# Kernel tuning notes

Measured on AMD Instinct MI355X. Metric: run time of the kernel, lower is better.

The kernel has to match this reference:

```python
import jax, jax.numpy as jnp
import numpy as np

D_MODEL = 2048
D_STATE = 16
BATCH = 2048

def setup_inputs() -> dict:
    key = jax.random.key(0)
    ks = jax.random.split(key, 8)
    x_t = jax.random.normal(ks[0], (BATCH, D_MODEL), dtype=jnp.float32)
    ssm_state_prev = jax.random.normal(ks[1], (BATCH, D_MODEL, D_STATE), dtype=jnp.float32)
    # parameters (match torch init semantics loosely; values random)
    A_log = jnp.log(jnp.tile(jnp.arange(1, D_STATE + 1, dtype=jnp.float32)[None, :], (D_MODEL, 1)))
    s = 1.0 / np.sqrt(D_MODEL)
    W_B = jax.random.uniform(ks[2], (D_STATE, D_MODEL), minval=-s, maxval=s, dtype=jnp.float32)
    W_C = jax.random.uniform(ks[3], (D_STATE, D_MODEL), minval=-s, maxval=s, dtype=jnp.float32)
    W_Delta = jax.random.uniform(ks[4], (D_MODEL, D_MODEL), minval=-s, maxval=s, dtype=jnp.float32)
    b_Delta = jax.random.uniform(ks[5], (D_MODEL,), minval=-s, maxval=s, dtype=jnp.float32)
    D_param = jnp.ones((D_MODEL,), dtype=jnp.float32)
    return {"x_t": x_t, "ssm_state_prev": ssm_state_prev, "A_log": A_log,
            "W_B": W_B, "W_C": W_C, "W_Delta": W_Delta, "b_Delta": b_Delta,
            "D_param": D_param}

def reference(x_t, ssm_state_prev, A_log, W_B, W_C, W_Delta, b_Delta, D_param):
    A = -jnp.exp(A_log)                         # (d_model, d_state)
    B_t = x_t @ W_B.T                            # (B, d_state)
    C_t = x_t @ W_C.T                            # (B, d_state)
    Delta_t = jax.nn.softplus(x_t @ W_Delta.T + b_Delta)   # (B, d_model)
    A_bar = jnp.exp(Delta_t[:, :, None] * A[None, :, :])   # (B, d_model, d_state)
    Delta_B = Delta_t[:, :, None] * B_t[:, None, :]         # (B, d_model, d_state)
    ssm_state_t = A_bar * ssm_state_prev + Delta_B * x_t[:, :, None]
    y_t = jnp.sum(ssm_state_t * C_t[:, None, :], axis=-1) + D_param * x_t
    return (y_t, ssm_state_t)
```

## Files before the change

kernel.cpp:

```cpp
#include <hip/hip_runtime.h>

#define D_MODEL 2048
#define D_STATE 16
#define BATCH   2048

typedef __attribute__((ext_vector_type(8))) short bf16x8;
typedef __attribute__((ext_vector_type(4))) float f32x4;
typedef __attribute__((ext_vector_type(8))) unsigned short u16x8;

__device__ __forceinline__ unsigned short f2bf(float f) {
  unsigned u = __float_as_uint(f);
  u = (u + 0x7FFFu + ((u >> 16) & 1u)) >> 16;
  return (unsigned short)u;
}

__device__ __forceinline__ void cvt8(const float* __restrict__ s, unsigned short* __restrict__ d) {
  f32x4 a = *(const f32x4*)s;
  f32x4 b = *(const f32x4*)(s + 4);
  u16x8 o;
  o[0] = f2bf(a[0]); o[1] = f2bf(a[1]); o[2] = f2bf(a[2]); o[3] = f2bf(a[3]);
  o[4] = f2bf(b[0]); o[5] = f2bf(b[1]); o[6] = f2bf(b[2]); o[7] = f2bf(b[3]);
  *(u16x8*)d = o;
}

__global__ __launch_bounds__(256) void prep_kernel(
    const float* __restrict__ x, const float* __restrict__ wd,
    const float* __restrict__ wb, const float* __restrict__ wc,
    const float* __restrict__ alog,
    unsigned short* __restrict__ x_bf, unsigned short* __restrict__ w_bf,
    unsigned short* __restrict__ wbc, float* __restrict__ nA) {
  int t = blockIdx.x * 256 + threadIdx.x;
  if (t < 524288) {
    cvt8(x + t * 8, x_bf + t * 8);
  } else if (t < 1048576) {
    int i = (t - 524288) * 8;
    cvt8(wd + i, w_bf + i);
  } else if (t < 1081344) {
    int i = (t - 1048576) * 8;
    int row = i >> 11, col = i & 2047;
    if (row < 16)      cvt8(wb + row * 2048 + col, wbc + i);
    else if (row < 32) cvt8(wc + (row - 16) * 2048 + col, wbc + i);
    else { u16x8 z = {0,0,0,0,0,0,0,0}; *(u16x8*)(wbc + i) = z; }
  } else {
    int i = (t - 1081344) * 4;
    f32x4 v = *(const f32x4*)(alog + i);
    f32x4 o;
    o[0] = __expf(v[0]); o[1] = __expf(v[1]); o[2] = __expf(v[2]); o[3] = __expf(v[3]);
    *(f32x4*)(nA + i) = o;
  }
}

__global__ __launch_bounds__(256) void gemm_kernel(
    const unsigned short* __restrict__ Abf,
    const unsigned short* __restrict__ Wbf,
    const unsigned short* __restrict__ WBC,
    const float* __restrict__ bias,
    float* __restrict__ Delta,
    float* __restrict__ BC) {
  __shared__ __align__(16) unsigned short lA[2][8192];
  __shared__ __align__(16) unsigned short lB[2][8192];

  const int tid = threadIdx.x;
  const bool isBC = (blockIdx.y == 16);
  const int brow = blockIdx.x * 128;
  const int bcol = isBC ? 0 : blockIdx.y * 128;
  const unsigned short* Bsrc = isBC ? WBC : (Wbf + (size_t)bcol * 2048);
  const unsigned short* Asrc = Abf + (size_t)brow * 2048;

  const int lane = tid & 63;
  const int wid = tid >> 6;
  const int wr = wid >> 1, wcid = wid & 1;
  const int fr = lane & 15;
  const int kg = lane >> 4;

  int srcoff[4];
#pragma unroll
  for (int i = 0; i < 4; ++i) {
    int ci = i * 256 + tid;
    int r = ci >> 3, cs = ci & 7;
    int c = cs ^ (r & 7);
    srcoff[i] = r * 2048 + c * 8;
  }
  const int ldsb = (tid >> 6) << 10;

  f32x4 acc[4][4];
#pragma unroll
  for (int m = 0; m < 4; ++m)
#pragma unroll
    for (int n = 0; n < 4; ++n) acc[m][n] = (f32x4){0.f, 0.f, 0.f, 0.f};

#define STAGE(buf, k0)                                                          \
  do {                                                                          \
    _Pragma("unroll")                                                           \
    for (int i = 0; i < 4; ++i)                                                 \
      __builtin_amdgcn_global_load_lds(                                         \
          (const __attribute__((address_space(1))) void*)(Asrc + (size_t)srcoff[i] + (k0)), \
          (__attribute__((address_space(3))) void*)((char*)lA[buf] + i * 4096 + ldsb), \
          16, 0, 0);                                                            \
    _Pragma("unroll")                                                           \
    for (int i = 0; i < 4; ++i)                                                 \
      __builtin_amdgcn_global_load_lds(                                         \
          (const __attribute__((address_space(1))) void*)(Bsrc + (size_t)srcoff[i] + (k0)), \
          (__attribute__((address_space(3))) void*)((char*)lB[buf] + i * 4096 + ldsb), \
          16, 0, 0);                                                            \
  } while (0)

  STAGE(0, 0);
  asm volatile("s_waitcnt vmcnt(0)" ::: "memory");
  __builtin_amdgcn_s_barrier();
  int cur = 0;
#pragma unroll 1
  for (int t = 0; t < 32; ++t) {
    if (t < 31) STAGE(cur ^ 1, (t + 1) * 64);

    bf16x8 fa[2][4], fb[2][4];
#pragma unroll
    for (int m = 0; m < 4; ++m) {
      int row = wr * 64 + m * 16 + fr;
#pragma unroll
      for (int kk = 0; kk < 2; ++kk)
        fa[kk][m] = *(const bf16x8*)((const char*)lA[cur] + row * 128 +
                                     ((((kk << 2) + kg) ^ (row & 7)) << 4));
    }
#pragma unroll
    for (int n = 0; n < 4; ++n) {
      int row = wcid * 64 + n * 16 + fr;
#pragma unroll
      for (int kk = 0; kk < 2; ++kk)
        fb[kk][n] = *(const bf16x8*)((const char*)lB[cur] + row * 128 +
                                     ((((kk << 2) + kg) ^ (row & 7)) << 4));
    }
#pragma unroll
    for (int kk = 0; kk < 2; ++kk)
#pragma unroll
      for (int m = 0; m < 4; ++m)
#pragma unroll
        for (int n = 0; n < 4; ++n)
          acc[m][n] = __builtin_amdgcn_mfma_f32_16x16x32_bf16(fa[kk][m], fb[kk][n], acc[m][n], 0, 0, 0);

    asm volatile("s_waitcnt vmcnt(0)" ::: "memory");
    __builtin_amdgcn_s_barrier();
    cur ^= 1;
  }
#undef STAGE

  const int rq = kg * 4;
#pragma unroll
  for (int m = 0; m < 4; ++m) {
    int grow = brow + wr * 64 + m * 16 + rq;
#pragma unroll
    for (int n = 0; n < 4; ++n) {
      int gcol = bcol + wcid * 64 + n * 16 + fr;
      if (!isBC) {
        float bv = bias[gcol];
#pragma unroll
        for (int q = 0; q < 4; ++q) {
          float v = acc[m][n][q] + bv;
          v = fmaxf(v, 0.f) + log1pf(__expf(-fabsf(v)));
          Delta[(size_t)(grow + q) * 2048 + gcol] = v;
        }
      } else {
#pragma unroll
        for (int q = 0; q < 4; ++q)
          BC[(size_t)(grow + q) * 128 + gcol] = acc[m][n][q];
      }
    }
  }
}

__global__ __launch_bounds__(256) void pointwise_kernel(
    const float* __restrict__ x, const float* __restrict__ sp,
    const float* __restrict__ nA, const float* __restrict__ BCb,
    const float* __restrict__ Delta, const float* __restrict__ Dp,
    float* __restrict__ y, float* __restrict__ st) {
  int t = blockIdx.x * 256 + threadIdx.x;
  int sg = t & 1;
  int d = (t >> 1) & 2047;
  int b = t >> 12;
  int bd = (b << 11) + d;
  float delta = Delta[bd];
  float xv = x[bd];
  float dx = delta * xv;
  const f32x4* spp = (const f32x4*)sp + ((size_t)t << 1);
  f32x4 s0 = __builtin_nontemporal_load(spp);
  f32x4 s1 = __builtin_nontemporal_load(spp + 1);
  const f32x4* ap = (const f32x4*)nA + ((d << 2) + (sg << 1));
  f32x4 a0 = ap[0], a1 = ap[1];
  const f32x4* bp = (const f32x4*)BCb + ((b << 5) + (sg << 1));
  f32x4 b0 = bp[0], b1 = bp[1];
  f32x4 c0 = bp[4], c1 = bp[5];
  f32x4 r0, r1;
  r0[0] = __expf(-delta * a0[0]) * s0[0] + dx * b0[0];
  r0[1] = __expf(-delta * a0[1]) * s0[1] + dx * b0[1];
  r0[2] = __expf(-delta * a0[2]) * s0[2] + dx * b0[2];
  r0[3] = __expf(-delta * a0[3]) * s0[3] + dx * b0[3];
  r1[0] = __expf(-delta * a1[0]) * s1[0] + dx * b1[0];
  r1[1] = __expf(-delta * a1[1]) * s1[1] + dx * b1[1];
  r1[2] = __expf(-delta * a1[2]) * s1[2] + dx * b1[2];
  r1[3] = __expf(-delta * a1[3]) * s1[3] + dx * b1[3];
  f32x4* stp = (f32x4*)st + ((size_t)t << 1);
  __builtin_nontemporal_store(r0, stp);
  __builtin_nontemporal_store(r1, stp + 1);
  float p = r0[0] * c0[0] + r0[1] * c0[1] + r0[2] * c0[2] + r0[3] * c0[3]
          + r1[0] * c1[0] + r1[1] * c1[1] + r1[2] * c1[2] + r1[3] * c1[3];
  p += __shfl_xor(p, 1, 2);
  if (sg == 0) y[bd] = p + Dp[d] * xv;
}

extern "C" void kernel_launch(void* const* d_in, const int* in_sizes, int n_in,
                              void* d_out, int out_size, void* d_ws, size_t ws_size,
                              hipStream_t stream) {
  const float* x    = (const float*)d_in[0];
  const float* sp   = (const float*)d_in[1];
  const float* alog = (const float*)d_in[2];
  const float* wb   = (const float*)d_in[3];
  const float* wc   = (const float*)d_in[4];
  const float* wd   = (const float*)d_in[5];
  const float* bdel = (const float*)d_in[6];
  const float* dp   = (const float*)d_in[7];
  float* y  = (float*)d_out;
  float* st = (float*)d_out + (size_t)BATCH * D_MODEL;

  char* ws = (char*)d_ws;
  unsigned short* x_bf = (unsigned short*)ws;
  unsigned short* w_bf = (unsigned short*)(ws + 8388608);
  unsigned short* wbc  = (unsigned short*)(ws + 16777216);
  float* Delta = (float*)(ws + 17301504);
  float* BC    = (float*)(ws + 34078720);
  float* nA    = (float*)(ws + 35127296);

  prep_kernel<<<4256, 256, 0, stream>>>(x, wd, wb, wc, alog, x_bf, w_bf, wbc, nA);
  gemm_kernel<<<dim3(16, 17), 256, 0, stream>>>(x_bf, w_bf, wbc, bdel, Delta, BC);
  pointwise_kernel<<<32768, 256, 0, stream>>>(x, sp, nA, BC, Delta, dp, y, st);
}
```

Baseline: 547.4 us.

## Fuse SSM pointwise update into GEMM epilogue and compute B/C projections in prep

```diff
diff --git a/kernel.cpp b/kernel.cpp
--- a/kernel.cpp
+++ b/kernel.cpp
@@ -28,44 +28,58 @@
     const float* __restrict__ wb, const float* __restrict__ wc,
     const float* __restrict__ alog,
     unsigned short* __restrict__ x_bf, unsigned short* __restrict__ w_bf,
-    unsigned short* __restrict__ wbc, float* __restrict__ nA) {
-  int t = blockIdx.x * 256 + threadIdx.x;
-  if (t < 524288) {
-    cvt8(x + t * 8, x_bf + t * 8);
-  } else if (t < 1048576) {
-    int i = (t - 524288) * 8;
+    float* __restrict__ nA, float* __restrict__ BCg) {
+  const int bid = blockIdx.x, tid = threadIdx.x;
+  if (bid < 2048) {
+    int i = (bid * 256 + tid) * 8;
+    cvt8(x + i, x_bf + i);
+  } else if (bid < 4096) {
+    int i = ((bid - 2048) * 256 + tid) * 8;
     cvt8(wd + i, w_bf + i);
-  } else if (t < 1081344) {
-    int i = (t - 1048576) * 8;
-    int row = i >> 11, col = i & 2047;
-    if (row < 16)      cvt8(wb + row * 2048 + col, wbc + i);
-    else if (row < 32) cvt8(wc + (row - 16) * 2048 + col, wbc + i);
-    else { u16x8 z = {0,0,0,0,0,0,0,0}; *(u16x8*)(wbc + i) = z; }
-  } else {
-    int i = (t - 1081344) * 4;
+  } else if (bid < 4128) {
+    int i = ((bid - 4096) * 256 + tid) * 4;
     f32x4 v = *(const f32x4*)(alog + i);
     f32x4 o;
     o[0] = __expf(v[0]); o[1] = __expf(v[1]); o[2] = __expf(v[2]); o[3] = __expf(v[3]);
     *(f32x4*)(nA + i) = o;
-  }
-}
-
-__global__ __launch_bounds__(256) void gemm_kernel(
+  } else {
+    int bci = bid - 4128;
+    int r = bci * 16 + (tid >> 4);
+    int j0 = (tid & 15) * 2;
+    const float* xr = x + (size_t)r * 2048;
+    const float* w0 = (j0 < 16) ? (wb + j0 * 2048) : (wc + (j0 - 16) * 2048);
+    const float* w1 = (j0 + 1 < 16) ? (wb + (j0 + 1) * 2048) : (wc + (j0 - 15) * 2048);
+    f32x4 a0 = (f32x4){0.f, 0.f, 0.f, 0.f}, a1 = a0;
+    for (int k = 0; k < 2048; k += 4) {
+      f32x4 xv = *(const f32x4*)(xr + k);
+      a0 += xv * *(const f32x4*)(w0 + k);
+      a1 += xv * *(const f32x4*)(w1 + k);
+    }
+    BCg[(size_t)r * 32 + j0]     = a0[0] + a0[1] + a0[2] + a0[3];
+    BCg[(size_t)r * 32 + j0 + 1] = a1[0] + a1[1] + a1[2] + a1[3];
+  }
+}
+
+#define LDSA(buf) ((unsigned short*)(smem + (buf) * 16384))
+#define LDSB(buf) ((unsigned short*)(smem + 32768 + (buf) * 16384))
+
+__global__ __launch_bounds__(256) void fused_kernel(
     const unsigned short* __restrict__ Abf,
     const unsigned short* __restrict__ Wbf,
-    const unsigned short* __restrict__ WBC,
     const float* __restrict__ bias,
-    float* __restrict__ Delta,
-    float* __restrict__ BC) {
-  __shared__ __align__(16) unsigned short lA[2][8192];
-  __shared__ __align__(16) unsigned short lB[2][8192];
+    const float* __restrict__ nAg,
+    const float* __restrict__ BCg,
+    const float* __restrict__ xg,
+    const float* __restrict__ sp,
+    const float* __restrict__ Dp,
+    float* __restrict__ y, float* __restrict__ st) {
+  __shared__ __align__(16) unsigned char smem[65536];
 
   const int tid = threadIdx.x;
-  const bool isBC = (blockIdx.y == 16);
   const int brow = blockIdx.x * 128;
-  const int bcol = isBC ? 0 : blockIdx.y * 128;
-  const unsigned short* Bsrc = isBC ? WBC : (Wbf + (size_t)bcol * 2048);
+  const int bcol = blockIdx.y * 128;
   const unsigned short* Asrc = Abf + (size_t)brow * 2048;
+  const unsigned short* Bsrc = Wbf + (size_t)bcol * 2048;
 
   const int lane = tid & 63;
   const int wid = tid >> 6;
@@ -95,13 +109,13 @@
     for (int i = 0; i < 4; ++i)                                                 \
       __builtin_amdgcn_global_load_lds(                                         \
           (const __attribute__((address_space(1))) void*)(Asrc + (size_t)srcoff[i] + (k0)), \
-          (__attribute__((address_space(3))) void*)((char*)lA[buf] + i * 4096 + ldsb), \
+          (__attribute__((address_space(3))) void*)((char*)LDSA(buf) + i * 4096 + ldsb), \
           16, 0, 0);                                                            \
     _Pragma("unroll")                                                           \
     for (int i = 0; i < 4; ++i)                                                 \
       __builtin_amdgcn_global_load_lds(                                         \
           (const __attribute__((address_space(1))) void*)(Bsrc + (size_t)srcoff[i] + (k0)), \
-          (__attribute__((address_space(3))) void*)((char*)lB[buf] + i * 4096 + ldsb), \
+          (__attribute__((address_space(3))) void*)((char*)LDSB(buf) + i * 4096 + ldsb), \
           16, 0, 0);                                                            \
   } while (0)
 
@@ -119,7 +133,7 @@
       int row = wr * 64 + m * 16 + fr;
 #pragma unroll
       for (int kk = 0; kk < 2; ++kk)
-        fa[kk][m] = *(const bf16x8*)((const char*)lA[cur] + row * 128 +
+        fa[kk][m] = *(const bf16x8*)((const char*)LDSA(cur) + row * 128 +
                                      ((((kk << 2) + kg) ^ (row & 7)) << 4));
     }
 #pragma unroll
@@ -127,7 +141,7 @@
       int row = wcid * 64 + n * 16 + fr;
 #pragma unroll
       for (int kk = 0; kk < 2; ++kk)
-        fb[kk][n] = *(const bf16x8*)((const char*)lB[cur] + row * 128 +
+        fb[kk][n] = *(const bf16x8*)((const char*)LDSB(cur) + row * 128 +
                                      ((((kk << 2) + kg) ^ (row & 7)) << 4));
     }
 #pragma unroll
@@ -144,67 +158,86 @@
   }
 #undef STAGE
 
-  const int rq = kg * 4;
+  float bvn[4], dpn[4];
+#pragma unroll
+  for (int n = 0; n < 4; ++n) {
+    int gcol = bcol + wcid * 64 + n * 16 + fr;
+    bvn[n] = bias[gcol];
+    dpn[n] = Dp[gcol];
+  }
+#pragma unroll
+  for (int m = 0; m < 4; ++m)
+#pragma unroll
+    for (int n = 0; n < 4; ++n)
+#pragma unroll
+      for (int q = 0; q < 4; ++q) {
+        float v = acc[m][n][q] + bvn[n];
+        acc[m][n][q] = fmaxf(v, 0.f) + log1pf(__expf(-fabsf(v)));
+      }
+
+  __syncthreads();
+  float* bc_lds = (float*)smem;
+  float* na_lds = (float*)(smem + 16384);
+  {
+    const f32x4* src = (const f32x4*)(BCg + (size_t)brow * 32);
+#pragma unroll
+    for (int i = 0; i < 4; ++i) ((f32x4*)bc_lds)[tid + i * 256] = src[tid + i * 256];
+    const float* ns = nAg + (size_t)bcol * 16;
+#pragma unroll
+    for (int i = 0; i < 8; ++i) {
+      int idx = tid + i * 256;
+      na_lds[(idx >> 4) * 20 + (idx & 15)] = ns[idx];
+    }
+  }
+  __syncthreads();
+
+  f32x4 na_reg[4][4];
+#pragma unroll
+  for (int n = 0; n < 4; ++n) {
+    const float* np = na_lds + (wcid * 64 + n * 16 + fr) * 20;
+#pragma unroll
+    for (int s = 0; s < 4; ++s) na_reg[n][s] = *(const f32x4*)(np + s * 4);
+  }
+
 #pragma unroll
   for (int m = 0; m < 4; ++m) {
-    int grow = brow + wr * 64 + m * 16 + rq;
-#pragma unroll
-    for (int n = 0; n < 4; ++n) {
-      int gcol = bcol + wcid * 64 + n * 16 + fr;
-      if (!isBC) {
-        float bv = bias[gcol];
-#pragma unroll
-        for (int q = 0; q < 4; ++q) {
-          float v = acc[m][n][q] + bv;
-          v = fmaxf(v, 0.f) + log1pf(__expf(-fabsf(v)));
-          Delta[(size_t)(grow + q) * 2048 + gcol] = v;
+#pragma unroll
+    for (int q = 0; q < 4; ++q) {
+      int bloc = wr * 64 + m * 16 + (kg << 2) + q;
+      int bglob = brow + bloc;
+      const float* bcp = bc_lds + bloc * 32;
+      f32x4 bt[4], ct[4];
+#pragma unroll
+      for (int s = 0; s < 4; ++s) {
+        bt[s] = *(const f32x4*)(bcp + s * 4);
+        ct[s] = *(const f32x4*)(bcp + 16 + s * 4);
+      }
+      size_t rowbase = (size_t)bglob << 11;
+#pragma unroll
+      for (int n = 0; n < 4; ++n) {
+        int dglob = bcol + wcid * 64 + n * 16 + fr;
+        float delta = acc[m][n][q];
+        float xv = xg[rowbase + dglob];
+        float dx = delta * xv;
+        const f32x4* spp = (const f32x4*)sp + ((rowbase + dglob) << 2);
+        f32x4* stp = (f32x4*)st + ((rowbase + dglob) << 2);
+        float psum = 0.f;
+#pragma unroll
+        for (int s = 0; s < 4; ++s) {
+          f32x4 sv = __builtin_nontemporal_load(spp + s);
+          f32x4 av = na_reg[n][s];
+          f32x4 r;
+          r[0] = __expf(-delta * av[0]) * sv[0] + dx * bt[s][0];
+          r[1] = __expf(-delta * av[1]) * sv[1] + dx * bt[s][1];
+          r[2] = __expf(-delta * av[2]) * sv[2] + dx * bt[s][2];
+          r[3] = __expf(-delta * av[3]) * sv[3] + dx * bt[s][3];
+          __builtin_nontemporal_store(r, stp + s);
+          psum += r[0] * ct[s][0] + r[1] * ct[s][1] + r[2] * ct[s][2] + r[3] * ct[s][3];
         }
-      } else {
-#pragma unroll
-        for (int q = 0; q < 4; ++q)
-          BC[(size_t)(grow + q) * 128 + gcol] = acc[m][n][q];
+        y[rowbase + dglob] = psum + dpn[n] * xv;
       }
     }
   }
-}
-
-__global__ __launch_bounds__(256) void pointwise_kernel(
-    const float* __restrict__ x, const float* __restrict__ sp,
-    const float* __restrict__ nA, const float* __restrict__ BCb,
-    const float* __restrict__ Delta, const float* __restrict__ Dp,
-    float* __restrict__ y, float* __restrict__ st) {
-  int t = blockIdx.x * 256 + threadIdx.x;
-  int sg = t & 1;
-  int d = (t >> 1) & 2047;
-  int b = t >> 12;
-  int bd = (b << 11) + d;
-  float delta = Delta[bd];
-  float xv = x[bd];
-  float dx = delta * xv;
-  const f32x4* spp = (const f32x4*)sp + ((size_t)t << 1);
-  f32x4 s0 = __builtin_nontemporal_load(spp);
-  f32x4 s1 = __builtin_nontemporal_load(spp + 1);
-  const f32x4* ap = (const f32x4*)nA + ((d << 2) + (sg << 1));
-  f32x4 a0 = ap[0], a1 = ap[1];
-  const f32x4* bp = (const f32x4*)BCb + ((b << 5) + (sg << 1));
-  f32x4 b0 = bp[0], b1 = bp[1];
-  f32x4 c0 = bp[4], c1 = bp[5];
-  f32x4 r0, r1;
-  r0[0] = __expf(-delta * a0[0]) * s0[0] + dx * b0[0];
-  r0[1] = __expf(-delta * a0[1]) * s0[1] + dx * b0[1];
-  r0[2] = __expf(-delta * a0[2]) * s0[2] + dx * b0[2];
-  r0[3] = __expf(-delta * a0[3]) * s0[3] + dx * b0[3];
-  r1[0] = __expf(-delta * a1[0]) * s1[0] + dx * b1[0];
-  r1[1] = __expf(-delta * a1[1]) * s1[1] + dx * b1[1];
-  r1[2] = __expf(-delta * a1[2]) * s1[2] + dx * b1[2];
-  r1[3] = __expf(-delta * a1[3]) * s1[3] + dx * b1[3];
-  f32x4* stp = (f32x4*)st + ((size_t)t << 1);
-  __builtin_nontemporal_store(r0, stp);
-  __builtin_nontemporal_store(r1, stp + 1);
-  float p = r0[0] * c0[0] + r0[1] * c0[1] + r0[2] * c0[2] + r0[3] * c0[3]
-          + r1[0] * c1[0] + r1[1] * c1[1] + r1[2] * c1[2] + r1[3] * c1[3];
-  p += __shfl_xor(p, 1, 2);
-  if (sg == 0) y[bd] = p + Dp[d] * xv;
 }
 
 extern "C" void kernel_launch(void* const* d_in, const int* in_sizes, int n_in,
@@ -224,12 +257,9 @@
   char* ws = (char*)d_ws;
   unsigned short* x_bf = (unsigned short*)ws;
   unsigned short* w_bf = (unsigned short*)(ws + 8388608);
-  unsigned short* wbc  = (unsigned short*)(ws + 16777216);
-  float* Delta = (float*)(ws + 17301504);
-  float* BC    = (float*)(ws + 34078720);
-  float* nA    = (float*)(ws + 35127296);
-
-  prep_kernel<<<4256, 256, 0, stream>>>(x, wd, wb, wc, alog, x_bf, w_bf, wbc, nA);
-  gemm_kernel<<<dim3(16, 17), 256, 0, stream>>>(x_bf, w_bf, wbc, bdel, Delta, BC);
-  pointwise_kernel<<<32768, 256, 0, stream>>>(x, sp, nA, BC, Delta, dp, y, st);
-}
+  float* nA  = (float*)(ws + 16777216);
+  float* BCg = (float*)(ws + 16908288);
+
+  prep_kernel<<<4256, 256, 0, stream>>>(x, wd, wb, wc, alog, x_bf, w_bf, nA, BCg);
+  fused_kernel<<<dim3(16, 16), 256, 0, stream>>>(x_bf, w_bf, bdel, nA, BCg, x, sp, dp, y, st);
+}
```

Result: slower. 1.384 ms (+152.9%).
